# Kernel optimization log

Hardware: AMD Instinct MI355X
Metric: run time of the kernel (lower is better)

## Reference

```python
import jax, jax.numpy as jnp
import numpy as np

NEG_INF = -1000000.0
B_, NG, HEADS, C, GH, GW, GD = 256, 64, 6, 192, 6, 6, 6
N = GH * GW * GD
POS_DIM = (C // 4) // 4  # DynamicPosBias(dim//4): pos_dim = (dim//4)//4 = 12


def setup_inputs() -> dict:
    key = jax.random.key(0)
    ks = jax.random.split(key, 12)
    rn = lambda k, shape, s=0.02: jax.random.normal(k, shape, jnp.float32) * s
    x = jax.random.normal(ks[0], (B_, N, C), jnp.float32)
    y = jax.random.normal(ks[1], (B_, N, C), jnp.float32)
    # 0 / -1e6 window mask, as produced by the padding logic upstream
    mask = jnp.where(jax.random.bernoulli(ks[2], 0.1, (NG, N, N)), NEG_INF, 0.0).astype(jnp.float32)
    return dict(
        x=x, y=y, mask=mask,
        Wqkv=rn(ks[3], (3 * C, C)), bqkv=jnp.zeros((3 * C,), jnp.float32),
        Wproj=rn(ks[4], (C, C)), bproj=jnp.zeros((C,), jnp.float32),
        pos_proj_w=rn(ks[5], (POS_DIM, 3)), pos_proj_b=jnp.zeros((POS_DIM,), jnp.float32),
        ln1_g=jnp.ones((POS_DIM,), jnp.float32), ln1_b=jnp.zeros((POS_DIM,), jnp.float32),
        pos1_w=rn(ks[6], (POS_DIM, POS_DIM)), pos1_b=jnp.zeros((POS_DIM,), jnp.float32),
        ln2_g=jnp.ones((POS_DIM,), jnp.float32), ln2_b=jnp.zeros((POS_DIM,), jnp.float32),
        pos2_w=rn(ks[7], (POS_DIM, POS_DIM)), pos2_b=jnp.zeros((POS_DIM,), jnp.float32),
        ln3_g=jnp.ones((POS_DIM,), jnp.float32), ln3_b=jnp.zeros((POS_DIM,), jnp.float32),
        pos3_w=rn(ks[8], (HEADS, POS_DIM)), pos3_b=jnp.zeros((HEADS,), jnp.float32),
        H=GH, W=GW, D=GD)


def _ln(t, g, b):
    m = t.mean(-1, keepdims=True)
    v = ((t - m) ** 2).mean(-1, keepdims=True)
    return (t - m) / jnp.sqrt(v + 1e-5) * g + b


def _rel_tables(H, W, D):
    # biases: all relative offsets in [1-H,H-1]x[1-W,W-1]x[1-D,D-1], shape (M, 3)
    ph = np.arange(1 - H, H); pw = np.arange(1 - W, W); pd = np.arange(1 - D, D)
    biases = np.stack(np.meshgrid(ph, pw, pd, indexing='ij')).reshape(3, -1).T.astype(np.float32)
    coords = np.stack(np.meshgrid(np.arange(H), np.arange(W), np.arange(D), indexing='ij')).reshape(3, -1)
    rel = (coords[:, :, None] - coords[:, None, :]).transpose(1, 2, 0)  # (N, N, 3)
    rel[..., 0] += H - 1; rel[..., 1] += W - 1; rel[..., 2] += D - 1
    rel[..., 0] *= (2 * W - 1) * (2 * D - 1); rel[..., 1] *= (2 * D - 1)
    idx = rel.sum(-1)  # (N, N) indices into the (M,) bias table
    return jnp.asarray(biases), jnp.asarray(idx)


def reference(x, y, mask, Wqkv, bqkv, Wproj, bproj, pos_proj_w, pos_proj_b,
              ln1_g, ln1_b, pos1_w, pos1_b, ln2_g, ln2_b, pos2_w, pos2_b,
              ln3_g, ln3_b, pos3_w, pos3_b, H, W, D):
    Bt, n, c = x.shape
    heads = pos3_w.shape[0]
    hd = c // heads
    scale = hd ** (-0.5)
    # NOTE: original code applies self.qkv to BOTH x and y (qkv_y layer unused)
    qkv = (x @ Wqkv.T + bqkv).reshape(Bt, n, 3, heads, hd).transpose(2, 0, 3, 1, 4)
    qkv_y = (y @ Wqkv.T + bqkv).reshape(Bt, n, 3, heads, hd).transpose(2, 0, 3, 1, 4)
    q = qkv[0] * scale
    k_y, v_y = qkv_y[1], qkv_y[2]
    attn = jnp.einsum('bhnd,bhmd->bhnm', q, k_y)
    # dynamic relative position bias: tiny MLP over offsets, then gather
    biases, idx = _rel_tables(H, W, D)
    pos = biases @ pos_proj_w.T + pos_proj_b
    pos = jnp.maximum(_ln(pos, ln1_g, ln1_b), 0) @ pos1_w.T + pos1_b
    pos = jnp.maximum(_ln(pos, ln2_g, ln2_b), 0) @ pos2_w.T + pos2_b
    pos = jnp.maximum(_ln(pos, ln3_g, ln3_b), 0) @ pos3_w.T + pos3_b  # (M, heads)
    rpb = pos[idx.reshape(-1)].reshape(n, n, heads).transpose(2, 0, 1)  # (heads, N, N)
    attn = attn + rpb[None]
    nG = mask.shape[0]
    attn = attn.reshape(Bt // nG, nG, heads, n, n) + mask[None, :, None]
    attn = jax.nn.softmax(attn, axis=-1).reshape(Bt, heads, n, n)
    out = jnp.einsum('bhnm,bhmd->bhnd', attn, v_y).transpose(0, 2, 1, 3).reshape(Bt, n, c)
    return out @ Wproj.T + bproj
```

## Files before the change

### kernel.cpp

```cpp
#include <hip/hip_runtime.h>
#include <stdint.h>

using short8   = __attribute__((ext_vector_type(8))) short;
using short4_  = __attribute__((ext_vector_type(4))) short;
using float4_  = __attribute__((ext_vector_type(4))) float;
using ushort4_ = __attribute__((ext_vector_type(4))) unsigned short;
typedef unsigned int  uint;
typedef unsigned short ushort;

__device__ __forceinline__ float bf2f(ushort b) {
  uint u = ((uint)b) << 16;
  return __builtin_bit_cast(float, u);
}
__device__ __forceinline__ ushort f2bf(float f) {
  uint u = __builtin_bit_cast(uint, f);
  u = u + 0x7fffu + ((u >> 16) & 1u);
  return (ushort)(u >> 16);
}

#define NN   216
#define NSQ  46656
#define PADV (-3.0e6f)

#if __has_builtin(__builtin_amdgcn_mfma_f32_16x16x16bf16_1k)
  #define HAVE_MFMA16 1
  #define MFMA16(a, b, c) __builtin_amdgcn_mfma_f32_16x16x16bf16_1k(a, b, c, 0, 0, 0)
#elif __has_builtin(__builtin_amdgcn_mfma_f32_16x16x16_bf16)
  #define HAVE_MFMA16 1
  #define MFMA16(a, b, c) __builtin_amdgcn_mfma_f32_16x16x16_bf16(a, b, c, 0, 0, 0)
#else
  #define HAVE_MFMA16 0
#endif

#define WA_WQKV   0
#define WA_BQKV   110592
#define WA_WPROJ  111168
#define WA_BPROJ  148032
#define WA_PPW    148224
#define WA_PPB    148260
#define WA_G1     148272
#define WA_B1     148284
#define WA_W1     148296
#define WA_WB1    148440
#define WA_G2     148452
#define WA_B2     148464
#define WA_W2     148476
#define WA_WB2    148620
#define WA_G3     148632
#define WA_B3     148644
#define WA_W3     148656
#define WA_WB3    148728
#define WA_TOTAL  148740

__global__ void detect_kernel(const uint* __restrict__ x, int* __restrict__ flag) {
  int lane = threadIdx.x;
  uint w = x[lane];
  ushort lo = (ushort)(w & 0xffffu);
  int e = (lo >> 7) & 0xff;
  int sane = (lo == 0 || (e >= 0x60 && e <= 0x9f)) ? 1 : 0;
  unsigned long long b = __ballot(sane);
  if (lane == 0) flag[0] = (__popcll(b) >= 56) ? 0 : 1;
}

struct SrcPtrs { const void* p[18]; };

__global__ void convert_kernel(SrcPtrs sp, ushort* __restrict__ dst,
                               const int* __restrict__ flag) {
  constexpr int OFF[19] = {WA_WQKV, WA_BQKV, WA_WPROJ, WA_BPROJ, WA_PPW, WA_PPB,
                           WA_G1, WA_B1, WA_W1, WA_WB1, WA_G2, WA_B2, WA_W2,
                           WA_WB2, WA_G3, WA_B3, WA_W3, WA_WB3, WA_TOTAL};
  int t = blockIdx.x * 256 + threadIdx.x;
  if (t >= WA_TOTAL) return;
  int a = 0;
#pragma unroll
  for (int i = 1; i < 18; ++i) a += (t >= OFF[i]) ? 1 : 0;
  int local = t - OFF[a];
  const void* s = sp.p[a];
  ushort v;
  if (flag[0]) v = f2bf(((const float*)s)[local]);
  else         v = ((const ushort*)s)[local];
  dst[t] = v;
}

__global__ __launch_bounds__(256) void cvt_kernel(const float* __restrict__ src,
                                                  ushort* __restrict__ dst,
                                                  const int* __restrict__ flag) {
  if (flag[0] == 0) return;
  size_t s = ((size_t)blockIdx.x * 256 + threadIdx.x) * 8;
  float4_ lo = *(const float4_*)(src + s);
  float4_ hi = *(const float4_*)(src + s + 4);
  short8 pk;
#pragma unroll
  for (int j = 0; j < 4; ++j) {
    pk[j]     = (short)f2bf(lo[j]);
    pk[4 + j] = (short)f2bf(hi[j]);
  }
  *(short8*)(dst + s) = pk;
}

__device__ __forceinline__ void ln_relu(const float* p, const ushort* g,
                                        const ushort* b, float* r) {
  float m = 0.f;
#pragma unroll
  for (int t = 0; t < 12; ++t) m += p[t];
  m *= (1.f / 12.f);
  float v = 0.f;
#pragma unroll
  for (int t = 0; t < 12; ++t) { float d = p[t] - m; v += d * d; }
  v *= (1.f / 12.f);
  float inv = rsqrtf(v + 1e-5f);
#pragma unroll
  for (int t = 0; t < 12; ++t) {
    float z = (p[t] - m) * inv * bf2f(g[t]) + bf2f(b[t]);
    r[t] = fmaxf(z, 0.f);
  }
}

__global__ void pos_mlp_kernel(const ushort* __restrict__ wa, float* __restrict__ pos) {
  int m = blockIdx.x * blockDim.x + threadIdx.x;
  if (m >= 1331) return;
  const ushort* pw  = wa + WA_PPW;  const ushort* pb  = wa + WA_PPB;
  const ushort* g1  = wa + WA_G1;   const ushort* b1  = wa + WA_B1;
  const ushort* w1  = wa + WA_W1;   const ushort* wb1 = wa + WA_WB1;
  const ushort* g2  = wa + WA_G2;   const ushort* b2  = wa + WA_B2;
  const ushort* w2  = wa + WA_W2;   const ushort* wb2 = wa + WA_WB2;
  const ushort* g3  = wa + WA_G3;   const ushort* b3  = wa + WA_B3;
  const ushort* w3  = wa + WA_W3;   const ushort* wb3 = wa + WA_WB3;

  int ih = m / 121, rem = m - ih * 121;
  int iw = rem / 11, id = rem - iw * 11;
  float fh = (float)(ih - 5), fw = (float)(iw - 5), fd = (float)(id - 5);
  float p[12], r[12], q[12];
#pragma unroll
  for (int t = 0; t < 12; ++t)
    p[t] = fh * bf2f(pw[t * 3]) + fw * bf2f(pw[t * 3 + 1]) +
           fd * bf2f(pw[t * 3 + 2]) + bf2f(pb[t]);
  ln_relu(p, g1, b1, r);
#pragma unroll
  for (int t = 0; t < 12; ++t) {
    float s = bf2f(wb1[t]);
#pragma unroll
    for (int u = 0; u < 12; ++u) s += r[u] * bf2f(w1[t * 12 + u]);
    q[t] = s;
  }
  ln_relu(q, g2, b2, r);
#pragma unroll
  for (int t = 0; t < 12; ++t) {
    float s = bf2f(wb2[t]);
#pragma unroll
    for (int u = 0; u < 12; ++u) s += r[u] * bf2f(w2[t * 12 + u]);
    p[t] = s;
  }
  ln_relu(p, g3, b3, r);
#pragma unroll
  for (int h = 0; h < 6; ++h) {
    float s = bf2f(wb3[h]);
#pragma unroll
    for (int u = 0; u < 12; ++u) s += r[u] * bf2f(w3[h * 12 + u]);
    pos[m * 6 + h] = s;
  }
}

__global__ void rpbfrag_kernel(const float* __restrict__ pos, ushort* __restrict__ out) {
  int tgl = blockIdx.x * 256 + threadIdx.x;
  if (tgl >= 6 * 196 * 64) return;
  int lane = tgl & 63;
  int tj   = (tgl >> 6) % 196;
  int h    = (tgl >> 6) / 196;
  int tt = tj / 14, jt = tj - tt * 14;
  int l16 = lane & 15, quad = lane >> 4;
  int i = tt * 16 + l16;
  int jbase = jt * 16 + quad * 4;
  ushort4_ o;
  if (i < 216 && jbase < 216) {
    int h1 = i / 36, r1 = i - h1 * 36, w1 = r1 / 6, d1 = r1 - w1 * 6;
#pragma unroll
    for (int r = 0; r < 4; ++r) {
      int j = jbase + r;
      int h2 = j / 36, r2 = j - h2 * 36, w2 = r2 / 6, d2 = r2 - w2 * 6;
      int idx = ((h1 - h2 + 5) * 11 + (w1 - w2 + 5)) * 11 + (d1 - d2 + 5);
      o[r] = f2bf(pos[idx * 6 + h]);
    }
  } else {
#pragma unroll
    for (int r = 0; r < 4; ++r) o[r] = f2bf(PADV);
  }
  *(ushort4_*)(out + (size_t)tgl * 4) = o;
}

__global__ void maskfrag_kernel(const void* __restrict__ maskv,
                                const int* __restrict__ flag,
                                ushort* __restrict__ out) {
  int tgl = blockIdx.x * 256 + threadIdx.x;
  if (tgl >= 64 * 196 * 64) return;
  bool mf32 = flag[0] != 0;
  int lane = tgl & 63;
  int tj   = (tgl >> 6) % 196;
  int g    = (tgl >> 6) / 196;
  int tt = tj / 14, jt = tj - tt * 14;
  int l16 = lane & 15, quad = lane >> 4;
  int i = tt * 16 + l16;
  int jbase = jt * 16 + quad * 4;
  ushort4_ o;
  if (i < 216 && jbase < 216) {
    int mi = i * 216 + jbase;
    if (mf32) {
      float4_ mv = *(const float4_*)((const float*)maskv + (size_t)g * NSQ + mi);
#pragma unroll
      for (int r = 0; r < 4; ++r) o[r] = f2bf(mv[r]);
    } else {
      o = *(const ushort4_*)((const ushort*)maskv + (size_t)g * NSQ + mi);
    }
  } else {
#pragma unroll
    for (int r = 0; r < 4; ++r) o[r] = f2bf(PADV);
  }
  *(ushort4_*)(out + (size_t)tgl * 4) = o;
}

__global__ __launch_bounds__(256, 2) void gemm_kernel(
    const void* __restrict__ p0,
    const ushort* __restrict__ p1,
    const void* __restrict__ p2,
    const ushort* __restrict__ W,  const ushort* __restrict__ bias,
    void* __restrict__ dq, void* __restrict__ dk, void* __restrict__ dv,
    const int* __restrict__ flag, int is_proj) {
  __shared__ __align__(16) ushort b_lds[2304 * 8];

  int tid = threadIdx.x;
  int m0 = blockIdx.x * 128;
  int n0 = blockIdx.y * 96;
  int z  = blockIdx.z;
  int wbase = is_proj ? 0 : z * 192;
  float scale = (!is_proj && z == 0) ? 0.17677669529663687f : 1.0f;
  void* dst = (z == 0) ? dq : (z == 1 ? dk : dv);
  int fl = flag[0];
  bool f32path = (!is_proj) && (z == 0) && (fl != 0);
  bool o_f32 = is_proj && (fl != 0);

  const ushort* A16;
  if (is_proj)      A16 = p1;
  else if (z == 0)  A16 = (const ushort*)p0;
  else              A16 = fl ? p1 : (const ushort*)p2;
  const float* A32 = (const float*)p0;

  int lane = tid & 63, w = tid >> 6;
  int l16 = lane & 15, quad = lane >> 4;

  short8 af[6][2];
  if (f32path) {
    float4_ a32[6][2][2];
#pragma unroll
    for (int kk = 0; kk < 6; ++kk)
#pragma unroll
      for (int mt = 0; mt < 2; ++mt) {
        const float* Af = A32 + (size_t)(m0 + w * 32 + mt * 16 + l16) * 192 + kk * 32 + quad * 8;
        a32[kk][mt][0] = *(const float4_*)Af;
        a32[kk][mt][1] = *(const float4_*)(Af + 4);
      }
#pragma unroll
    for (int kk = 0; kk < 6; ++kk)
#pragma unroll
      for (int mt = 0; mt < 2; ++mt)
#pragma unroll
        for (int j = 0; j < 4; ++j) {
          af[kk][mt][j]     = (short)f2bf(a32[kk][mt][0][j]);
          af[kk][mt][4 + j] = (short)f2bf(a32[kk][mt][1][j]);
        }
  } else {
#pragma unroll
    for (int kk = 0; kk < 6; ++kk)
#pragma unroll
      for (int mt = 0; mt < 2; ++mt)
        af[kk][mt] = *(const short8*)(A16 + (size_t)(m0 + w * 32 + mt * 16 + l16) * 192 + kk * 32 + quad * 8);
  }

#pragma unroll
  for (int it = 0; it < 9; ++it) {
    int s = tid + it * 256;
    int kk = s / 384;
    int rem = s - kk * 384;
    int nt = rem >> 6;
    int l  = rem & 63;
    int l16v = l & 15, qv = l >> 4;
    short8 pk = *(const short8*)(W + (size_t)(wbase + n0 + nt * 16 + l16v) * 192 + kk * 32 + qv * 8);
    *(short8*)(b_lds + s * 8) = pk;
  }
  __syncthreads();

  float4_ acc[2][6];
#pragma unroll
  for (int mt = 0; mt < 2; ++mt)
#pragma unroll
    for (int nt = 0; nt < 6; ++nt) acc[mt][nt] = (float4_){0.f, 0.f, 0.f, 0.f};

#pragma unroll
  for (int kk = 0; kk < 6; ++kk) {
    short8 bfr[6];
#pragma unroll
    for (int nt = 0; nt < 6; ++nt)
      bfr[nt] = *(const short8*)(b_lds + ((kk * 6 + nt) * 64 + lane) * 8);
#pragma unroll
    for (int mt = 0; mt < 2; ++mt)
#pragma unroll
      for (int nt = 0; nt < 6; ++nt)
        acc[mt][nt] = __builtin_amdgcn_mfma_f32_16x16x32_bf16(af[kk][mt], bfr[nt], acc[mt][nt], 0, 0, 0);
  }

#pragma unroll
  for (int mt = 0; mt < 2; ++mt) {
#pragma unroll
    for (int nt = 0; nt < 6; ++nt) {
      int lcol = n0 + nt * 16 + l16;
      float bv = bf2f(bias[(is_proj ? 0 : z * 192) + lcol]);
#pragma unroll
      for (int r = 0; r < 4; ++r) {
        int grow = m0 + w * 32 + mt * 16 + quad * 4 + r;
        float val = (acc[mt][nt][r] + bv) * scale;
        if (is_proj) {
          if (o_f32) ((float*)dst)[(size_t)grow * 192 + lcol] = val;
          else       ((ushort*)dst)[(size_t)grow * 192 + lcol] = f2bf(val);
        } else {
          int bb = grow / 216;
          int nn2 = grow - bb * 216;
          int hh = lcol >> 5, dd = lcol & 31;
          ((ushort*)dst)[(((size_t)bb * 6 + hh) * 216 + nn2) * 32 + dd] = f2bf(val);
        }
      }
    }
  }
}

__global__ __launch_bounds__(256) void attn_kernel(
    const ushort* __restrict__ q, const ushort* __restrict__ k,
    const ushort* __restrict__ v, const ushort* __restrict__ rpbf,
    const ushort* __restrict__ maskf, ushort* __restrict__ opre) {
#if HAVE_MFMA16
  __shared__ __align__(16) ushort vfrag[28 * 64 * 4];
#else
  __shared__ __align__(16) ushort vfrag[14 * 64 * 8];
#endif

  int bid = blockIdx.x;
  int b = bid / 6, h = bid - b * 6;
  int g = b & 63;
  int tid = threadIdx.x, lane = tid & 63, w = tid >> 6;
  int l16 = lane & 15, quad = lane >> 4;

  const ushort* qh = q + (size_t)(b * 6 + h) * 6912;
  const ushort* kh = k + (size_t)(b * 6 + h) * 6912;
  const ushort* vh = v + (size_t)(b * 6 + h) * 6912;

#if HAVE_MFMA16
  for (int pos = tid; pos < 1792; pos += 256) {
    int chunk = pos >> 6, l = pos & 63;
    int kt = chunk >> 1, dh = chunk & 1;
    int qd = l >> 4, lv = l & 15;
    ushort4_ tmp;
#pragma unroll
    for (int j = 0; j < 4; ++j)
      tmp[j] = vh[(kt * 16 + qd * 4 + j) * 32 + dh * 16 + lv];
    *(ushort4_*)(vfrag + pos * 4) = tmp;
  }
#else
  for (int pos = tid; pos < 896; pos += 256) {
    int chunk = pos >> 6, l = pos & 63;
    int kt2 = chunk >> 1, dh = chunk & 1;
    int qd = l >> 4, lv = l & 15;
    short8 tmp;
#pragma unroll
    for (int j = 0; j < 8; ++j)
      tmp[j] = (short)vh[(kt2 * 32 + qd * 8 + j) * 32 + dh * 16 + lv];
    *(short8*)(vfrag + pos * 8) = tmp;
  }
#endif
  __syncthreads();

  for (int t = w; t < 14; t += 4) {
    int r0 = t * 16;
    const ushort* rf = rpbf  + ((size_t)(h * 196 + t * 14) * 64 + lane) * 4;
    const ushort* mf = maskf + ((size_t)(g * 196 + t * 14) * 64 + lane) * 4;
    short8 aq = *(const short8*)(qh + (r0 + l16) * 32 + quad * 8);

    float4_ st[14];
#pragma unroll
    for (int jt = 0; jt < 14; ++jt) {
      ushort4_ rb = *(const ushort4_*)(rf + jt * 256);
      ushort4_ mb = *(const ushort4_*)(mf + jt * 256);
      float4_ cin;
#pragma unroll
      for (int r = 0; r < 4; ++r) cin[r] = bf2f(rb[r]) + bf2f(mb[r]);
      short8 bk = *(const short8*)(kh + (jt * 16 + l16) * 32 + quad * 8);
      st[jt] = __builtin_amdgcn_mfma_f32_16x16x32_bf16(bk, aq, cin, 0, 0, 0);
    }

    float mx = -1e30f;
#pragma unroll
    for (int jt = 0; jt < 14; ++jt)
#pragma unroll
      for (int r = 0; r < 4; ++r) mx = fmaxf(mx, st[jt][r]);
    mx = fmaxf(mx, __shfl_xor(mx, 16));
    mx = fmaxf(mx, __shfl_xor(mx, 32));
    float sum = 0.f;
#pragma unroll
    for (int jt = 0; jt < 14; ++jt)
#pragma unroll
      for (int r = 0; r < 4; ++r) {
        float pe = __expf(st[jt][r] - mx);
        st[jt][r] = pe;
        sum += pe;
      }
    sum += __shfl_xor(sum, 16);
    sum += __shfl_xor(sum, 32);
    float inv = 1.0f / sum;

    float4_ o0 = (float4_){0.f, 0.f, 0.f, 0.f};
    float4_ o1 = (float4_){0.f, 0.f, 0.f, 0.f};

#if HAVE_MFMA16
#pragma unroll
    for (int kt = 0; kt < 14; ++kt) {
      short4_ pa;
#pragma unroll
      for (int r = 0; r < 4; ++r) pa[r] = (short)f2bf(st[kt][r]);
      short4_ vb0 = *(const short4_*)(vfrag + ((kt * 2 + 0) * 64 + lane) * 4);
      short4_ vb1 = *(const short4_*)(vfrag + ((kt * 2 + 1) * 64 + lane) * 4);
      o0 = MFMA16(pa, vb0, o0);
      o1 = MFMA16(pa, vb1, o1);
    }
#else
#pragma unroll
    for (int kt2 = 0; kt2 < 7; ++kt2) {
      uint pe0 = ((uint)f2bf(st[2*kt2][0])) | (((uint)f2bf(st[2*kt2][1])) << 16);
      uint pe1 = ((uint)f2bf(st[2*kt2][2])) | (((uint)f2bf(st[2*kt2][3])) << 16);
      uint po0 = ((uint)f2bf(st[2*kt2+1][0])) | (((uint)f2bf(st[2*kt2+1][1])) << 16);
      uint po1 = ((uint)f2bf(st[2*kt2+1][2])) | (((uint)f2bf(st[2*kt2+1][3])) << 16);
      int slo = (((2 * quad) & 3) << 4) | l16;
      int shi = (((2 * quad + 1) & 3) << 4) | l16;
      uint e_lo0 = __shfl((int)pe0, slo), e_lo1 = __shfl((int)pe1, slo);
      uint o_lo0 = __shfl((int)po0, slo), o_lo1 = __shfl((int)po1, slo);
      uint e_hi0 = __shfl((int)pe0, shi), e_hi1 = __shfl((int)pe1, shi);
      uint o_hi0 = __shfl((int)po0, shi), o_hi1 = __shfl((int)po1, shi);
      uint lo0 = (quad < 2) ? e_lo0 : o_lo0, lo1 = (quad < 2) ? e_lo1 : o_lo1;
      uint hi0 = (quad < 2) ? e_hi0 : o_hi0, hi1 = (quad < 2) ? e_hi1 : o_hi1;
      uint4 paw = {lo0, lo1, hi0, hi1};
      short8 pa = __builtin_bit_cast(short8, paw);
      short8 vb0 = *(const short8*)(vfrag + ((kt2 * 2 + 0) * 64 + lane) * 8);
      short8 vb1 = *(const short8*)(vfrag + ((kt2 * 2 + 1) * 64 + lane) * 8);
      o0 = __builtin_amdgcn_mfma_f32_16x16x32_bf16(pa, vb0, o0, 0, 0, 0);
      o1 = __builtin_amdgcn_mfma_f32_16x16x32_bf16(pa, vb1, o1, 0, 0, 0);
    }
#endif

#pragma unroll
    for (int r = 0; r < 4; ++r) {
      float ir = __shfl(inv, quad * 4 + r);
      int i = r0 + quad * 4 + r;
      if (i < 216) {
        size_t base = ((size_t)b * 216 + i) * 192 + h * 32;
        opre[base + l16]      = f2bf(o0[r] * ir);
        opre[base + 16 + l16] = f2bf(o1[r] * ir);
      }
    }
  }
}

extern "C" void kernel_launch(void* const* d_in, const int* in_sizes, int n_in,
                              void* d_out, int out_size, void* d_ws, size_t ws_size,
                              hipStream_t stream) {
  (void)in_sizes; (void)n_in; (void)out_size; (void)ws_size;

  char* p = (char*)d_ws;
  int*    flag   = (int*)p;            p += 256;
  ushort* warena = (ushort*)p;         p += 298240;
  float*  pos    = (float*)p;          p += 32768;
  ushort* rpbf   = (ushort*)p;         p += 602112;
  ushort* maskf  = (ushort*)p;         p += 6422528;
  ushort* ycvt   = (ushort*)p;         p += 21234688;
  ushort* qb     = (ushort*)p;         p += 21234688;
  ushort* kb     = (ushort*)p;         p += 21234688;
  ushort* vb     = (ushort*)p;
  ushort* opre   = ycvt;

  detect_kernel<<<1, 64, 0, stream>>>((const uint*)d_in[0], flag);

  SrcPtrs sp;
  for (int i = 0; i < 18; ++i) sp.p[i] = d_in[3 + i];
  convert_kernel<<<(WA_TOTAL + 255) / 256, 256, 0, stream>>>(sp, warena, flag);

  cvt_kernel<<<5184, 256, 0, stream>>>((const float*)d_in[1], ycvt, flag);

  pos_mlp_kernel<<<6, 256, 0, stream>>>(warena, pos);
  rpbfrag_kernel<<<294, 256, 0, stream>>>(pos, rpbf);
  maskfrag_kernel<<<3136, 256, 0, stream>>>(d_in[2], flag, maskf);

  gemm_kernel<<<dim3(432, 2, 3), 256, 0, stream>>>(
      d_in[0], ycvt, d_in[1], warena + WA_WQKV, warena + WA_BQKV,
      qb, kb, vb, flag, 0);

  attn_kernel<<<1536, 256, 0, stream>>>(qb, kb, vb, rpbf, maskf, opre);

  gemm_kernel<<<dim3(432, 2, 1), 256, 0, stream>>>(
      opre, opre, opre, warena + WA_WPROJ, warena + WA_BPROJ,
      d_out, d_out, d_out, flag, 1);
}
```

Before: 303.3 us.

## Prepack y activations and weights into MFMA fragment order; fuse pos MLP into rpb

Converts y into a fragment-packed layout so the K/V GEMM loads A operands contiguously per tile. Qkv/proj weights are prepacked once so the GEMM LDS fill becomes a straight coalesced copy. The positional MLP is recomputed inside each rpbfrag block into shared memory, removing a kernel launch and the global pos buffer. In exchange it adds redundant MLP compute per block and an extra pack kernel.

```diff
diff --git a/kernel.cpp b/kernel.cpp
--- a/kernel.cpp
+++ b/kernel.cpp
@@ -82,20 +82,44 @@
   dst[t] = v;
 }
 
-__global__ __launch_bounds__(256) void cvt_kernel(const float* __restrict__ src,
-                                                  ushort* __restrict__ dst,
-                                                  const int* __restrict__ flag) {
-  if (flag[0] == 0) return;
-  size_t s = ((size_t)blockIdx.x * 256 + threadIdx.x) * 8;
-  float4_ lo = *(const float4_*)(src + s);
-  float4_ hi = *(const float4_*)(src + s + 4);
+__global__ void packw_kernel(const ushort* __restrict__ wa, ushort* __restrict__ wp) {
+  int c = blockIdx.x * 256 + threadIdx.x;
+  if (c >= 8 * 2304) return;
+  int blob = c / 2304, s = c - blob * 2304;
+  int kk = s / 384, r = s - kk * 384;
+  int nt = r >> 6, l = r & 63;
+  int l16 = l & 15, qd = l >> 4;
+  int col, base;
+  if (blob < 6) { int z = blob >> 1, half = blob & 1;
+                  col = z * 192 + half * 96 + nt * 16 + l16; base = WA_WQKV; }
+  else          { col = (blob - 6) * 96 + nt * 16 + l16;     base = WA_WPROJ; }
+  short8 pk = *(const short8*)(wa + base + (size_t)col * 192 + kk * 32 + qd * 8);
+  *(short8*)(wp + (size_t)c * 8) = pk;
+}
+
+__global__ __launch_bounds__(256) void packa_kernel(const void* __restrict__ src,
+                                                    ushort* __restrict__ dst,
+                                                    const int* __restrict__ flag) {
+  int c = blockIdx.x * 256 + threadIdx.x;
+  int tile = c / 3072, cc = c - tile * 3072;
+  int kk = cc / 512, c2 = cc - kk * 512;
+  int rowhi = c2 / 64, c3 = c2 - rowhi * 64;
+  int q = c3 >> 4, l16 = c3 & 15;
+  size_t M = (size_t)tile * 128 + rowhi * 16 + l16;
+  size_t so = M * 192 + kk * 32 + q * 8;
   short8 pk;
-#pragma unroll
-  for (int j = 0; j < 4; ++j) {
-    pk[j]     = (short)f2bf(lo[j]);
-    pk[4 + j] = (short)f2bf(hi[j]);
-  }
-  *(short8*)(dst + s) = pk;
+  if (flag[0]) {
+    float4_ lo = *(const float4_*)((const float*)src + so);
+    float4_ hi = *(const float4_*)((const float*)src + so + 4);
+#pragma unroll
+    for (int j = 0; j < 4; ++j) {
+      pk[j]     = (short)f2bf(lo[j]);
+      pk[4 + j] = (short)f2bf(hi[j]);
+    }
+  } else {
+    pk = *(const short8*)((const ushort*)src + so);
+  }
+  *(short8*)(dst + (size_t)c * 8) = pk;
 }
 
 __device__ __forceinline__ void ln_relu(const float* p, const ushort* g,
@@ -116,9 +140,7 @@
   }
 }
 
-__global__ void pos_mlp_kernel(const ushort* __restrict__ wa, float* __restrict__ pos) {
-  int m = blockIdx.x * blockDim.x + threadIdx.x;
-  if (m >= 1331) return;
+__device__ void pos_mlp_row(const ushort* wa, int m, float* out6) {
   const ushort* pw  = wa + WA_PPW;  const ushort* pb  = wa + WA_PPB;
   const ushort* g1  = wa + WA_G1;   const ushort* b1  = wa + WA_B1;
   const ushort* w1  = wa + WA_W1;   const ushort* wb1 = wa + WA_WB1;
@@ -126,7 +148,6 @@
   const ushort* w2  = wa + WA_W2;   const ushort* wb2 = wa + WA_WB2;
   const ushort* g3  = wa + WA_G3;   const ushort* b3  = wa + WA_B3;
   const ushort* w3  = wa + WA_W3;   const ushort* wb3 = wa + WA_WB3;
-
   int ih = m / 121, rem = m - ih * 121;
   int iw = rem / 11, id = rem - iw * 11;
   float fh = (float)(ih - 5), fw = (float)(iw - 5), fd = (float)(id - 5);
@@ -157,11 +178,21 @@
     float s = bf2f(wb3[h]);
 #pragma unroll
     for (int u = 0; u < 12; ++u) s += r[u] * bf2f(w3[h * 12 + u]);
-    pos[m * 6 + h] = s;
-  }
-}
-
-__global__ void rpbfrag_kernel(const float* __restrict__ pos, ushort* __restrict__ out) {
+    out6[h] = s;
+  }
+}
+
+__global__ __launch_bounds__(256) void rpbfrag_kernel(const ushort* __restrict__ wa,
+                                                      ushort* __restrict__ out) {
+  __shared__ float pos_l[1331 * 6];
+  for (int m = threadIdx.x; m < 1331; m += 256) {
+    float o6[6];
+    pos_mlp_row(wa, m, o6);
+#pragma unroll
+    for (int h = 0; h < 6; ++h) pos_l[m * 6 + h] = o6[h];
+  }
+  __syncthreads();
+
   int tgl = blockIdx.x * 256 + threadIdx.x;
   if (tgl >= 6 * 196 * 64) return;
   int lane = tgl & 63;
@@ -179,7 +210,7 @@
       int j = jbase + r;
       int h2 = j / 36, r2 = j - h2 * 36, w2 = r2 / 6, d2 = r2 - w2 * 6;
       int idx = ((h1 - h2 + 5) * 11 + (w1 - w2 + 5)) * 11 + (d1 - d2 + 5);
-      o[r] = f2bf(pos[idx * 6 + h]);
+      o[r] = f2bf(pos_l[idx * 6 + h]);
     }
   } else {
 #pragma unroll
@@ -219,72 +250,70 @@
 }
 
 __global__ __launch_bounds__(256, 2) void gemm_kernel(
-    const void* __restrict__ p0,
-    const ushort* __restrict__ p1,
-    const void* __restrict__ p2,
-    const ushort* __restrict__ W,  const ushort* __restrict__ bias,
+    const void* __restrict__ Arow,
+    const ushort* __restrict__ Apack,
+    const ushort* __restrict__ wpacked,
+    const ushort* __restrict__ bias,
     void* __restrict__ dq, void* __restrict__ dk, void* __restrict__ dv,
     const int* __restrict__ flag, int is_proj) {
   __shared__ __align__(16) ushort b_lds[2304 * 8];
 
   int tid = threadIdx.x;
-  int m0 = blockIdx.x * 128;
-  int n0 = blockIdx.y * 96;
+  int tile = blockIdx.x;
+  int m0 = tile * 128;
+  int half = blockIdx.y;
+  int n0 = half * 96;
   int z  = blockIdx.z;
-  int wbase = is_proj ? 0 : z * 192;
+  int blob = is_proj ? (6 + half) : (z * 2 + half);
   float scale = (!is_proj && z == 0) ? 0.17677669529663687f : 1.0f;
   void* dst = (z == 0) ? dq : (z == 1 ? dk : dv);
   int fl = flag[0];
+  bool a_packed = (!is_proj) && (z != 0);
   bool f32path = (!is_proj) && (z == 0) && (fl != 0);
   bool o_f32 = is_proj && (fl != 0);
 
-  const ushort* A16;
-  if (is_proj)      A16 = p1;
-  else if (z == 0)  A16 = (const ushort*)p0;
-  else              A16 = fl ? p1 : (const ushort*)p2;
-  const float* A32 = (const float*)p0;
-
   int lane = tid & 63, w = tid >> 6;
   int l16 = lane & 15, quad = lane >> 4;
 
   short8 af[6][2];
-  if (f32path) {
-    float4_ a32[6][2][2];
+  if (a_packed) {
+    const ushort* tb = Apack + (size_t)tile * 24576 + lane * 8;
 #pragma unroll
     for (int kk = 0; kk < 6; ++kk)
 #pragma unroll
+      for (int mt = 0; mt < 2; ++mt)
+        af[kk][mt] = *(const short8*)(tb + kk * 4096 + (w * 2 + mt) * 512);
+  } else if (f32path) {
+#pragma unroll
+    for (int kk = 0; kk < 6; ++kk)
+#pragma unroll
       for (int mt = 0; mt < 2; ++mt) {
-        const float* Af = A32 + (size_t)(m0 + w * 32 + mt * 16 + l16) * 192 + kk * 32 + quad * 8;
-        a32[kk][mt][0] = *(const float4_*)Af;
-        a32[kk][mt][1] = *(const float4_*)(Af + 4);
+        const float* Af = (const float*)Arow +
+            (size_t)(m0 + w * 32 + mt * 16 + l16) * 192 + kk * 32 + quad * 8;
+        float4_ lo = *(const float4_*)Af;
+        float4_ hi = *(const float4_*)(Af + 4);
+#pragma unroll
+        for (int j = 0; j < 4; ++j) {
+          af[kk][mt][j]     = (short)f2bf(lo[j]);
+          af[kk][mt][4 + j] = (short)f2bf(hi[j]);
+        }
       }
+  } else {
 #pragma unroll
     for (int kk = 0; kk < 6; ++kk)
 #pragma unroll
       for (int mt = 0; mt < 2; ++mt)
-#pragma unroll
-        for (int j = 0; j < 4; ++j) {
-          af[kk][mt][j]     = (short)f2bf(a32[kk][mt][0][j]);
-          af[kk][mt][4 + j] = (short)f2bf(a32[kk][mt][1][j]);
-        }
-  } else {
-#pragma unroll
-    for (int kk = 0; kk < 6; ++kk)
-#pragma unroll
-      for (int mt = 0; mt < 2; ++mt)
-        af[kk][mt] = *(const short8*)(A16 + (size_t)(m0 + w * 32 + mt * 16 + l16) * 192 + kk * 32 + quad * 8);
-  }
-
-#pragma unroll
-  for (int it = 0; it < 9; ++it) {
-    int s = tid + it * 256;
-    int kk = s / 384;
-    int rem = s - kk * 384;
-    int nt = rem >> 6;
-    int l  = rem & 63;
-    int l16v = l & 15, qv = l >> 4;
-    short8 pk = *(const short8*)(W + (size_t)(wbase + n0 + nt * 16 + l16v) * 192 + kk * 32 + qv * 8);
-    *(short8*)(b_lds + s * 8) = pk;
+        af[kk][mt] = *(const short8*)((const ushort*)Arow +
+            (size_t)(m0 + w * 32 + mt * 16 + l16) * 192 + kk * 32 + quad * 8);
+  }
+
+  {
+    const ushort* wb = wpacked + (size_t)blob * 18432;
+#pragma unroll
+    for (int it = 0; it < 9; ++it) {
+      int s = tid + it * 256;
+      *(short8*)(b_lds + s * 8) = *(const short8*)(wb + s * 8);
+    }
   }
   __syncthreads();
 
@@ -471,36 +500,35 @@
   (void)in_sizes; (void)n_in; (void)out_size; (void)ws_size;
 
   char* p = (char*)d_ws;
-  int*    flag   = (int*)p;            p += 256;
-  ushort* warena = (ushort*)p;         p += 298240;
-  float*  pos    = (float*)p;          p += 32768;
-  ushort* rpbf   = (ushort*)p;         p += 602112;
-  ushort* maskf  = (ushort*)p;         p += 6422528;
-  ushort* ycvt   = (ushort*)p;         p += 21234688;
-  ushort* qb     = (ushort*)p;         p += 21234688;
-  ushort* kb     = (ushort*)p;         p += 21234688;
-  ushort* vb     = (ushort*)p;
-  ushort* opre   = ycvt;
+  int*    flag    = (int*)p;           p += 256;
+  ushort* warena  = (ushort*)p;        p += 298240;
+  ushort* wpacked = (ushort*)p;        p += 294912;
+  ushort* rpbf    = (ushort*)p;        p += 602112;
+  ushort* maskf   = (ushort*)p;        p += 6422528;
+  ushort* yf      = (ushort*)p;        p += 21234688;
+  ushort* qb      = (ushort*)p;        p += 21234688;
+  ushort* kb      = (ushort*)p;        p += 21234688;
+  ushort* vb      = (ushort*)p;
+  ushort* opre    = yf;
 
   detect_kernel<<<1, 64, 0, stream>>>((const uint*)d_in[0], flag);
 
   SrcPtrs sp;
   for (int i = 0; i < 18; ++i) sp.p[i] = d_in[3 + i];
   convert_kernel<<<(WA_TOTAL + 255) / 256, 256, 0, stream>>>(sp, warena, flag);
-
-  cvt_kernel<<<5184, 256, 0, stream>>>((const float*)d_in[1], ycvt, flag);
-
-  pos_mlp_kernel<<<6, 256, 0, stream>>>(warena, pos);
-  rpbfrag_kernel<<<294, 256, 0, stream>>>(pos, rpbf);
+  packw_kernel<<<72, 256, 0, stream>>>(warena, wpacked);
+
+  packa_kernel<<<5184, 256, 0, stream>>>(d_in[1], yf, flag);
+
+  rpbfrag_kernel<<<294, 256, 0, stream>>>(warena, rpbf);
   maskfrag_kernel<<<3136, 256, 0, stream>>>(d_in[2], flag, maskf);
 
   gemm_kernel<<<dim3(432, 2, 3), 256, 0, stream>>>(
-      d_in[0], ycvt, d_in[1], warena + WA_WQKV, warena + WA_BQKV,
-      qb, kb, vb, flag, 0);
+      d_in[0], yf, wpacked, warena + WA_BQKV, qb, kb, vb, flag, 0);
 
   attn_kernel<<<1536, 256, 0, stream>>>(qb, kb, vb, rpbf, maskf, opre);
 
   gemm_kernel<<<dim3(432, 2, 1), 256, 0, stream>>>(
-      opre, opre, opre, warena + WA_WPROJ, warena + WA_BPROJ,
+      opre, yf, wpacked, warena + WA_BPROJ,
       d_out, d_out, d_out, flag, 1);
 }
```

Result: slower. 374.8 us (+23.6%).
